# Optimization experiments

Hardware: AMD Instinct MI355X
Metric: run time of the kernel (lower is better)

The kernel has to match this reference:

```python
import jax, jax.numpy as jnp
import numpy as np

B = 1024
IN_H, IN_W = 128, 128
KH, KW = 10, 10
SH, SW = 5, 5
PH, PW = 2, 2
HP, WP = IN_H + 2 * PH, IN_W + 2 * PW          # padded dims: 132, 132
NKH = (IN_H - KH + 2 * PH) // SH + 1            # 25
NKW = (IN_W - KW + 2 * PW) // SW + 1            # 25
NK = NKH * NKW                                  # 625


def _build_weight_matrix(kernel_weights):
    """kernel_weights: [NK, KH, KW] -> sparse-structured dense [HP*WP, NK].
    Faithful to LocallyConnected2dV2._create_weight_matrix, vectorized."""
    i = jnp.arange(NK)
    start_i = (i // NKW) * SH                   # [NK]
    start_j = (i % NKW) * SW                    # [NK]
    # flat row index for each (kernel, k, l) tap in padded image
    rows = ((start_i[:, None, None] + jnp.arange(KH)[None, :, None]) * WP
            + start_j[:, None, None] + jnp.arange(KW)[None, None, :])  # [NK,KH,KW]
    rows = rows.reshape(NK, KH * KW)
    cols = i[:, None]                           # [NK,1] broadcasts over taps
    W = jnp.zeros((HP * WP, NK), dtype=kernel_weights.dtype)
    return W.at[rows, cols].set(kernel_weights.reshape(NK, KH * KW))


def setup_inputs() -> dict:
    key = jax.random.key(0)
    kx, kw, kb = jax.random.split(key, 3)
    x = jax.random.normal(kx, (B, IN_H, IN_W), dtype=jnp.float32)
    kernel_weights = jax.random.normal(kw, (NK, KH, KW), dtype=jnp.float32)
    W = _build_weight_matrix(kernel_weights)    # [HP*WP, NK]
    bias = jax.random.normal(kb, (NKH, NKW), dtype=jnp.float32)
    return {"x": x, "W": W, "bias": bias}


def reference(x, W, bias):
    # zero-pad spatial dims, flatten, dense GEMM against sparse-structured W
    xp = jnp.pad(x, ((0, 0), (PH, PH), (PW, PW)))          # [B,HP,WP]
    xf = xp.reshape(x.shape[0], HP * WP)                   # [B,HP*WP]
    out = xf @ W                                           # [B,NK]
    out = out.reshape(x.shape[0], NKH, NKW)
    return out + bias
```

## Files before the change

### kernel.cpp

```cpp
#include <hip/hip_runtime.h>

typedef _Float16 f16x2 __attribute__((ext_vector_type(2)));
typedef __fp16  fp16x2 __attribute__((ext_vector_type(2)));

constexpr int NKW  = 25, NK = 625;
constexpr int WPADR = 132;
constexpr int WPT   = 160;
constexpr int RST   = 35;
constexpr int MAXR  = 40;

union U2H { unsigned int u; f16x2 h; fp16x2 p; };

__global__ void gather_wp(const float* __restrict__ W, _Float16* __restrict__ wgpT) {
    int t = blockIdx.x * 256 + threadIdx.x;
    if (t >= NK * WPT) return;
    int k = t / WPT, p = t % WPT;
    int di = p >> 4, s = p & 15;
    int ki = k / NKW, kj = k % NKW;
    int o = (5 * kj + 2) & 3;
    int j = s - o;
    float val = 0.f;
    if (j >= 0 && j < 10)
        val = W[(size_t)((ki * 5 + di) * WPADR + kj * 5 + j) * NK + k];
    wgpT[((size_t)(p >> 3) * NK + k) * 8 + (p & 7)] = (_Float16)val;
}

__device__ __forceinline__ float dot2acc(unsigned int a, unsigned int b, float c) {
    U2H ua, ub; ua.u = a; ub.u = b;
#if __has_builtin(__builtin_amdgcn_fdot2)
    return __builtin_amdgcn_fdot2(ua.h, ub.h, c, false);
#else
    return c + (float)ua.h.x * (float)ub.h.x + (float)ua.h.y * (float)ub.h.y;
#endif
}

template <bool USE_WG>
__global__ __launch_bounds__(256, 3)
void lc2d_pair(const float* __restrict__ x, const _Float16* __restrict__ wgpT,
               const float* __restrict__ Wfull,
               const float* __restrict__ bias, float* __restrict__ out) {
    __shared__ uint2 xs[2 * MAXR * RST];

    const int pair    = blockIdx.x;
    const int quarter = blockIdx.y;
    const int K0   = quarter ? (1 + 6 * quarter) : 0;
    const int NKI  = quarter ? 6 : 7;
    const int NROWS = 5 * NKI + 5;
    const int NOUT  = NKI * NKW;
    const int tid  = threadIdx.x;

    const bool active = tid < NOUT;
    const int ki_l = tid / 25;
    const int kj   = tid - ki_l * 25;
    const int k    = (K0 + ki_l) * NKW + kj;

    uint4 wq[20];
    float bval = 0.f;
    if (active) {
        if (USE_WG) {
            const uint4* wt4 = reinterpret_cast<const uint4*>(wgpT);
#pragma unroll
            for (int j = 0; j < 20; ++j) wq[j] = wt4[(size_t)j * NK + k];
        } else {
            const int o = (5 * kj + 2) & 3;
#pragma unroll
            for (int j = 0; j < 20; ++j) {
                const int di = j >> 1, pb = (j & 1) * 8;
                unsigned int uu[4];
#pragma unroll
                for (int m = 0; m < 4; ++m) {
                    float f0 = 0.f, f1 = 0.f;
                    const int j0 = pb + 2 * m - o, j1 = pb + 2 * m + 1 - o;
                    const size_t rowb = (size_t)(((K0 + ki_l) * 5 + di) * WPADR + kj * 5);
                    if (j0 >= 0 && j0 < 10) f0 = Wfull[(rowb + j0) * NK + k];
                    if (j1 >= 0 && j1 < 10) f1 = Wfull[(rowb + j1) * NK + k];
                    U2H u; u.p = __builtin_amdgcn_cvt_pkrtz(f0, f1);
                    uu[m] = u.u;
                }
                wq[j] = make_uint4(uu[0], uu[1], uu[2], uu[3]);
            }
        }
        bval = bias[k];
    }

#pragma unroll
    for (int img = 0; img < 2; ++img) {
        const float* xb = x + ((size_t)(2 * pair + img) << 14);
        uint2* xd = xs + img * (MAXR * RST);
        for (int i = tid; i < NROWS * 2; i += 256)
            xd[(i >> 1) * RST + (i & 1) * 33] = make_uint2(0u, 0u);
        for (int i = tid; i < NROWS * 32; i += 256) {
            const int idx = i >> 5, q = (i & 31) + 1;
            const int r = 5 * K0 + idx - 2;
            uint2 val = make_uint2(0u, 0u);
            if (r >= 0 && r < 128) {
                const float4 v = *reinterpret_cast<const float4*>(
                    xb + (r << 7) + ((q - 1) << 2));
                U2H u0, u1;
                u0.p = __builtin_amdgcn_cvt_pkrtz(v.x, v.y);
                u1.p = __builtin_amdgcn_cvt_pkrtz(v.z, v.w);
                val.x = u0.u; val.y = u1.u;
            }
            xd[idx * RST + q] = val;
        }
    }
    __syncthreads();

    if (!active) return;

    const int woff = (5 * kj + 2) >> 2;
#pragma unroll
    for (int img = 0; img < 2; ++img) {
        const uint2* base = xs + img * (MAXR * RST) + (5 * ki_l) * RST + woff;
        float acc0 = bval, acc1 = 0.f;
#pragma unroll
        for (int d = 0; d < 10; ++d) {
            const uint2* rowp = base + d * RST;
            const uint2 a0 = rowp[0], a1 = rowp[1], a2 = rowp[2], a3 = rowp[3];
            const uint4 wA = wq[2 * d], wB = wq[2 * d + 1];
            acc0 = dot2acc(a0.x, wA.x, acc0);
            acc1 = dot2acc(a0.y, wA.y, acc1);
            acc0 = dot2acc(a1.x, wA.z, acc0);
            acc1 = dot2acc(a1.y, wA.w, acc1);
            acc0 = dot2acc(a2.x, wB.x, acc0);
            acc1 = dot2acc(a2.y, wB.y, acc1);
            acc0 = dot2acc(a3.x, wB.z, acc0);
            acc1 = dot2acc(a3.y, wB.w, acc1);
        }
        out[(size_t)(2 * pair + img) * NK + k] = acc0 + acc1;
    }
}

extern "C" void kernel_launch(void* const* d_in, const int* in_sizes, int n_in,
                              void* d_out, int out_size, void* d_ws, size_t ws_size,
                              hipStream_t stream) {
    const float* x    = (const float*)d_in[0];
    const float* W    = (const float*)d_in[1];
    const float* bias = (const float*)d_in[2];
    float* out = (float*)d_out;

    const dim3 grid(512, 4);
    if (ws_size >= (size_t)NK * WPT * sizeof(_Float16)) {
        _Float16* wgpT = (_Float16*)d_ws;
        gather_wp<<<(NK * WPT + 255) / 256, 256, 0, stream>>>(W, wgpT);
        lc2d_pair<true><<<grid, 256, 0, stream>>>(x, wgpT, W, bias, out);
    } else {
        lc2d_pair<false><<<grid, 256, 0, stream>>>(x, nullptr, W, bias, out);
    }
}
```

Measured before the change: 131.7 us.

## Pipeline 8 images per block with double-buffered LDS and 6 row slabs

Each block now processes 8 images instead of 2 and splits the output rows into 6 slabs instead of 4. The next image's input rows are loaded into registers while the current image is computed from a double-buffered shared-memory tile, so global load latency overlaps the dot-product work. Per-thread weights are reused across more images, which amortizes the weight gather. In exchange, fewer threads per block are active (125 or 100 of 256), the input rows that neighbouring slabs share are reloaded more often, and the grid has fewer blocks.

```diff
diff --git a/kernel.cpp b/kernel.cpp
--- a/kernel.cpp
+++ b/kernel.cpp
@@ -7,7 +7,9 @@
 constexpr int WPADR = 132;
 constexpr int WPT   = 160;
 constexpr int RST   = 35;
-constexpr int MAXR  = 40;
+constexpr int IMG   = 8;
+constexpr int NSLAB = 6;
+constexpr int MAXR  = 30;
 
 union U2H { unsigned int u; f16x2 h; fp16x2 p; };
 
@@ -36,18 +38,20 @@
 
 template <bool USE_WG>
 __global__ __launch_bounds__(256, 3)
-void lc2d_pair(const float* __restrict__ x, const _Float16* __restrict__ wgpT,
+void lc2d_pipe(const float* __restrict__ x, const _Float16* __restrict__ wgpT,
                const float* __restrict__ Wfull,
                const float* __restrict__ bias, float* __restrict__ out) {
-    __shared__ uint2 xs[2 * MAXR * RST];
+    __shared__ uint2 xs[2][MAXR * RST];
 
-    const int pair    = blockIdx.x;
-    const int quarter = blockIdx.y;
-    const int K0   = quarter ? (1 + 6 * quarter) : 0;
-    const int NKI  = quarter ? 6 : 7;
-    const int NROWS = 5 * NKI + 5;
-    const int NOUT  = NKI * NKW;
+    const int grp  = blockIdx.x;
+    const int slab = blockIdx.y;
+    const int K0   = slab ? (4 * slab + 1) : 0;
+    const int NKI  = slab ? 4 : 5;
+    const int R    = 5 * NKI + 5;
+    const int NOUT = NKI * NKW;
+    const int row0 = 5 * K0 - 2;
     const int tid  = threadIdx.x;
+    const int b0   = grp * IMG;
 
     const bool active = tid < NOUT;
     const int ki_l = tid / 25;
@@ -83,51 +87,71 @@
         bval = bias[k];
     }
 
+    for (int i = tid; i < 4 * R; i += 256)
+        xs[i & 1][(i >> 2) * RST + ((i >> 1) & 1) * 33] = make_uint2(0u, 0u);
+
+    auto stage_load = [&](int img, float4* tmp) {
+        const float* xb = x + ((size_t)(b0 + img) << 14);
 #pragma unroll
-    for (int img = 0; img < 2; ++img) {
-        const float* xb = x + ((size_t)(2 * pair + img) << 14);
-        uint2* xd = xs + img * (MAXR * RST);
-        for (int i = tid; i < NROWS * 2; i += 256)
-            xd[(i >> 1) * RST + (i & 1) * 33] = make_uint2(0u, 0u);
-        for (int i = tid; i < NROWS * 32; i += 256) {
-            const int idx = i >> 5, q = (i & 31) + 1;
-            const int r = 5 * K0 + idx - 2;
-            uint2 val = make_uint2(0u, 0u);
-            if (r >= 0 && r < 128) {
-                const float4 v = *reinterpret_cast<const float4*>(
-                    xb + (r << 7) + ((q - 1) << 2));
+        for (int t = 0; t < 4; ++t) {
+            const int i = tid + t * 256;
+            tmp[t] = make_float4(0.f, 0.f, 0.f, 0.f);
+            if (i < R * 32) {
+                const int idx = i >> 5, q = i & 31;
+                const int r = row0 + idx;
+                if (r >= 0 && r < 128)
+                    tmp[t] = *reinterpret_cast<const float4*>(xb + (r << 7) + (q << 2));
+            }
+        }
+    };
+    auto stage_write = [&](int buf, const float4* tmp) {
+#pragma unroll
+        for (int t = 0; t < 4; ++t) {
+            const int i = tid + t * 256;
+            if (i < R * 32) {
+                const int idx = i >> 5, q = (i & 31) + 1;
                 U2H u0, u1;
-                u0.p = __builtin_amdgcn_cvt_pkrtz(v.x, v.y);
-                u1.p = __builtin_amdgcn_cvt_pkrtz(v.z, v.w);
-                val.x = u0.u; val.y = u1.u;
+                u0.p = __builtin_amdgcn_cvt_pkrtz(tmp[t].x, tmp[t].y);
+                u1.p = __builtin_amdgcn_cvt_pkrtz(tmp[t].z, tmp[t].w);
+                xs[buf][idx * RST + q] = make_uint2(u0.u, u1.u);
             }
-            xd[idx * RST + q] = val;
         }
+    };
+
+    {
+        float4 tmp[4];
+        stage_load(0, tmp);
+        stage_write(0, tmp);
     }
     __syncthreads();
 
-    if (!active) return;
+    for (int i = 0; i < IMG; ++i) {
+        float4 tmp[4];
+        const bool more = (i + 1 < IMG);
+        if (more) stage_load(i + 1, tmp);
 
-    const int woff = (5 * kj + 2) >> 2;
+        if (active) {
+            const uint2* base = xs[i & 1] + (5 * ki_l) * RST + ((5 * kj + 2) >> 2);
+            float acc0 = bval, acc1 = 0.f;
 #pragma unroll
-    for (int img = 0; img < 2; ++img) {
-        const uint2* base = xs + img * (MAXR * RST) + (5 * ki_l) * RST + woff;
-        float acc0 = bval, acc1 = 0.f;
-#pragma unroll
-        for (int d = 0; d < 10; ++d) {
-            const uint2* rowp = base + d * RST;
-            const uint2 a0 = rowp[0], a1 = rowp[1], a2 = rowp[2], a3 = rowp[3];
-            const uint4 wA = wq[2 * d], wB = wq[2 * d + 1];
-            acc0 = dot2acc(a0.x, wA.x, acc0);
-            acc1 = dot2acc(a0.y, wA.y, acc1);
-            acc0 = dot2acc(a1.x, wA.z, acc0);
-            acc1 = dot2acc(a1.y, wA.w, acc1);
-            acc0 = dot2acc(a2.x, wB.x, acc0);
-            acc1 = dot2acc(a2.y, wB.y, acc1);
-            acc0 = dot2acc(a3.x, wB.z, acc0);
-            acc1 = dot2acc(a3.y, wB.w, acc1);
+            for (int d = 0; d < 10; ++d) {
+                const uint2* rowp = base + d * RST;
+                const uint2 a0 = rowp[0], a1 = rowp[1], a2 = rowp[2], a3 = rowp[3];
+                const uint4 wA = wq[2 * d], wB = wq[2 * d + 1];
+                acc0 = dot2acc(a0.x, wA.x, acc0);
+                acc1 = dot2acc(a0.y, wA.y, acc1);
+                acc0 = dot2acc(a1.x, wA.z, acc0);
+                acc1 = dot2acc(a1.y, wA.w, acc1);
+                acc0 = dot2acc(a2.x, wB.x, acc0);
+                acc1 = dot2acc(a2.y, wB.y, acc1);
+                acc0 = dot2acc(a3.x, wB.z, acc0);
+                acc1 = dot2acc(a3.y, wB.w, acc1);
+            }
+            out[(size_t)(b0 + i) * NK + k] = acc0 + acc1;
         }
-        out[(size_t)(2 * pair + img) * NK + k] = acc0 + acc1;
+
+        if (more) stage_write((i + 1) & 1, tmp);
+        __syncthreads();
     }
 }
 
@@ -139,12 +163,12 @@
     const float* bias = (const float*)d_in[2];
     float* out = (float*)d_out;
 
-    const dim3 grid(512, 4);
+    const dim3 grid(1024 / IMG, NSLAB);
     if (ws_size >= (size_t)NK * WPT * sizeof(_Float16)) {
         _Float16* wgpT = (_Float16*)d_ws;
         gather_wp<<<(NK * WPT + 255) / 256, 256, 0, stream>>>(W, wgpT);
-        lc2d_pair<true><<<grid, 256, 0, stream>>>(x, wgpT, W, bias, out);
+        lc2d_pipe<true><<<grid, 256, 0, stream>>>(x, wgpT, W, bias, out);
     } else {
-        lc2d_pair<false><<<grid, 256, 0, stream>>>(x, nullptr, W, bias, out);
+        lc2d_pipe<false><<<grid, 256, 0, stream>>>(x, nullptr, W, bias, out);
     }
 }
```

After: 123.5 us. -6.2%, faster.
